# Kernel tuning notes

Measured on AMD Instinct MI355X. Metric: run time of the kernel, lower is better.

The kernel has to match this reference:

```python
import jax, jax.numpy as jnp
import numpy as np


def setup_inputs() -> dict:
    key = jax.random.key(0)
    k1, k2, k3 = jax.random.split(key, 3)
    B, D, L = 32768, 1024, 2
    return {
        "x": jax.random.normal(k1, (B, D), dtype=jnp.float32),
        "local_angles": jax.random.normal(k2, (L, D), dtype=jnp.float32),
        "ent_angles": jax.random.normal(k3, (L, D // 2), dtype=jnp.float32),
    }


def _local_layer(out, angles):
    # Sequential chain of Givens rotations on column pairs (i, (i+1)%D).
    # Each step uses the already-updated columns, exactly like the torch loop
    # (out = out @ R.T  ==  rotate columns i and j of out).
    D = out.shape[1]
    idx = jnp.arange(D)

    def body(o, inp):
        i, theta = inp
        j = (i + 1) % D
        c, s = jnp.cos(theta), jnp.sin(theta)
        ci = jnp.take(o, i, axis=1)  # [B]
        cj = jnp.take(o, j, axis=1)  # [B]
        o = o.at[:, i].set(c * ci - s * cj)
        o = o.at[:, j].set(s * ci + c * cj)
        return o, None

    out, _ = jax.lax.scan(body, out, (idx, angles))
    return out


def _ent_layer(out, angles):
    # Entangler rotations act on disjoint pairs (2k, 2k+1) -> fully vectorized.
    B, D = out.shape
    p = out.reshape(B, D // 2, 2)
    c, s = jnp.cos(angles), jnp.sin(angles)  # [D//2]
    x0, x1 = p[..., 0], p[..., 1]
    return jnp.stack([c * x0 - s * x1, s * x0 + c * x1], axis=-1).reshape(B, D)


def reference(x, local_angles, ent_angles):
    out = x
    num_layers = local_angles.shape[0]
    for l in range(num_layers):
        out = _local_layer(out, local_angles[l])
        out = _ent_layer(out, ent_angles[l])
    return out
```

## Files before the change

### kernel.cpp

```cpp
#include <hip/hip_runtime.h>

#define D_DIM    1024
#define PER_LANE 16
#define NLAYER   2
#define NPAIR    8
#define WPB      4
#define ROWS_PW  8
#define NBUF     4

typedef float nf4 __attribute__((ext_vector_type(4)));

__device__ __forceinline__ int swz(int c) { return c ^ ((c >> 3) & 7); }

template<int CTRL, int RMASK>
__device__ __forceinline__ float dpp_mov(float src, float oldv) {
    return __int_as_float(__builtin_amdgcn_update_dpp(
        __float_as_int(oldv), __float_as_int(src), CTRL, RMASK, 0xF, false));
}

__global__ void angles_kernel(const float* __restrict__ la,
                              const float* __restrict__ ea,
                              float* __restrict__ tab) {
    int t  = blockIdx.x * blockDim.x + threadIdx.x;
    int nt = gridDim.x * blockDim.x;
    for (int i = t; i < NLAYER * D_DIM; i += nt) {
        float s, c; sincosf(la[i], &s, &c);
        tab[i] = c; tab[2048 + i] = s;
    }
    for (int i = t; i < NLAYER * (D_DIM / 2); i += nt) {
        float s, c; sincosf(ea[i], &s, &c);
        tab[4096 + i] = c; tab[5120 + i] = s;
    }
}

__global__ __launch_bounds__(256) void qent_kernel(
        const float* __restrict__ x,
        const float* __restrict__ tab,
        float* __restrict__ out, int B)
{
    const int lane  = threadIdx.x & 63;
    const int wid   = threadIdx.x >> 6;
    const int gwave = blockIdx.x * WPB + wid;

    __shared__ float4 tb[WPB][NBUF][256];
    __shared__ float2 lds_ces[NLAYER][NPAIR][64];

    for (int t = threadIdx.x; t < NLAYER * 512; t += 256) {
        int L = t >> 9, p = t & 511;
        int m = p >> 6, ln = p & 63;
        float2 cs;
        cs.x = tab[4096 + L * 512 + ln * 8 + m];
        cs.y = tab[5120 + L * 512 + ln * 8 + m];
        lds_ces[L][m][ln] = cs;
    }
    __syncthreads();

    float cl[NLAYER][PER_LANE], sl[NLAYER][PER_LANE];
    #pragma unroll
    for (int L = 0; L < NLAYER; ++L) {
        const float4* cp = reinterpret_cast<const float4*>(tab + L * D_DIM + lane * PER_LANE);
        const float4* sp = reinterpret_cast<const float4*>(tab + 2048 + L * D_DIM + lane * PER_LANE);
        #pragma unroll
        for (int q = 0; q < 4; ++q) {
            float4 c4 = cp[q], s4 = sp[q];
            cl[L][4*q+0] = c4.x; cl[L][4*q+1] = c4.y; cl[L][4*q+2] = c4.z; cl[L][4*q+3] = c4.w;
            sl[L][4*q+0] = s4.x; sl[L][4*q+1] = s4.y; sl[L][4*q+2] = s4.z; sl[L][4*q+3] = s4.w;
        }
    }

    const int l2 = lane ^ (lane >> 3);
    auto stage = [&](int b, int row) {
        const float* src = x + (size_t)row * D_DIM;
        #pragma unroll
        for (int q = 0; q < 4; ++q) {
            __builtin_amdgcn_global_load_lds(
                (const __attribute__((address_space(1))) void*)(src + q * 256 + l2 * 4),
                (__attribute__((address_space(3))) void*)&tb[wid][b][q * 64],
                16, 0, 0);
        }
    };

    const int row0 = gwave * ROWS_PW;
    stage(0, row0 + 0);
    stage(1, row0 + 1);
    stage(2, row0 + 2);

    for (int it = 0; it < ROWS_PW; ++it) {
        const int cur = it & (NBUF - 1);

        if (it + 3 < ROWS_PW) stage((it + 3) & (NBUF - 1), row0 + it + 3);

        if      (it == 0)           asm volatile("s_waitcnt vmcnt(12)" ::: "memory");
        else if (it == 1)           asm volatile("s_waitcnt vmcnt(16)" ::: "memory");
        else if (it == 2)           asm volatile("s_waitcnt vmcnt(20)" ::: "memory");
        else if (it <= ROWS_PW - 4) asm volatile("s_waitcnt vmcnt(24)" ::: "memory");
        else if (it == ROWS_PW - 3) asm volatile("s_waitcnt vmcnt(20)" ::: "memory");
        else if (it == ROWS_PW - 2) asm volatile("s_waitcnt vmcnt(16)" ::: "memory");
        else                        asm volatile("s_waitcnt vmcnt(12)" ::: "memory");

        float v[PER_LANE];
        #pragma unroll
        for (int r = 0; r < 4; ++r) {
            float4 t = tb[wid][cur][swz(4 * lane + r)];
            v[4*r+0] = t.x; v[4*r+1] = t.y; v[4*r+2] = t.z; v[4*r+3] = t.w;
        }

        #pragma unroll
        for (int L = 0; L < NLAYER; ++L) {
            float vnf = dpp_mov<0x130, 0xF>(v[0], v[0]);

            float A = 1.f, Bv = 0.f;
            #pragma unroll
            for (int k = 0; k < PER_LANE; ++k) {
                float vn = (k < PER_LANE - 1) ? v[k + 1] : vnf;
                Bv = sl[L][k] * Bv + cl[L][k] * vn;
                A  = sl[L][k] * A;
            }

            float Ai = A, Bi = Bv;
            #define SCAN_STEP(CTRL, RMASK) do {                   \
                float Au = dpp_mov<CTRL, RMASK>(Ai, 1.0f);        \
                float Bu = dpp_mov<CTRL, RMASK>(Bi, 0.0f);        \
                Bi = fmaf(Ai, Bu, Bi);                            \
                Ai *= Au; } while (0)
            SCAN_STEP(0x111, 0xF);
            SCAN_STEP(0x112, 0xF);
            SCAN_STEP(0x114, 0xF);
            SCAN_STEP(0x118, 0xF);
            SCAN_STEP(0x142, 0xA);
            SCAN_STEP(0x143, 0xC);
            #undef SCAN_STEP

            float Ax = dpp_mov<0x138, 0xF>(Ai, 0.0f);
            float Bx = dpp_mov<0x138, 0xF>(Bi, 0.0f);
            float v0b = __int_as_float(
                __builtin_amdgcn_readfirstlane(__float_as_int(v[0])));
            float u   = (lane == 0) ? v[0] : fmaf(Ax, v0b, Bx);

            #pragma unroll
            for (int k = 0; k < PER_LANE - 1; ++k) {
                float vn = v[k + 1];
                float f  = cl[L][k] * u - sl[L][k] * vn;
                u        = sl[L][k] * u + cl[L][k] * vn;
                v[k] = f;
            }
            float a0 = __int_as_float(
                __builtin_amdgcn_readfirstlane(__float_as_int(v[0])));
            float vn15 = (lane == 63) ? a0 : vnf;
            float f15  = cl[L][PER_LANE-1] * u - sl[L][PER_LANE-1] * vn15;
            float un   = sl[L][PER_LANE-1] * u + cl[L][PER_LANE-1] * vn15;
            v[PER_LANE-1] = f15;
            float f0new = __int_as_float(
                __builtin_amdgcn_readlane(__float_as_int(un), 63));
            v[0] = (lane == 0) ? f0new : v[0];

            #pragma unroll
            for (int m = 0; m < NPAIR; ++m) {
                float2 cs = lds_ces[L][m][lane];
                float x0 = v[2*m], x1 = v[2*m+1];
                v[2*m]   = cs.x * x0 - cs.y * x1;
                v[2*m+1] = cs.y * x0 + cs.x * x1;
            }
        }

        #pragma unroll
        for (int r = 0; r < 4; ++r) {
            float4 t;
            t.x = v[4*r+0]; t.y = v[4*r+1]; t.z = v[4*r+2]; t.w = v[4*r+3];
            tb[wid][cur][swz(4 * lane + r)] = t;
        }
        nf4* op = reinterpret_cast<nf4*>(out + (size_t)(row0 + it) * D_DIM);
        #pragma unroll
        for (int q = 0; q < 4; ++q) {
            float4 t = tb[wid][cur][swz(q * 64 + lane)];
            nf4 w; w.x = t.x; w.y = t.y; w.z = t.z; w.w = t.w;
            __builtin_nontemporal_store(w, &op[q * 64 + lane]);
        }
    }
}

extern "C" void kernel_launch(void* const* d_in, const int* in_sizes, int n_in,
                              void* d_out, int out_size, void* d_ws, size_t ws_size,
                              hipStream_t stream) {
    const float* x  = (const float*)d_in[0];
    const float* la = (const float*)d_in[1];
    const float* ea = (const float*)d_in[2];
    float* out = (float*)d_out;
    float* tab = (float*)d_ws;
    int B = in_sizes[0] / D_DIM;

    angles_kernel<<<64, 256, 0, stream>>>(la, ea, tab);
    qent_kernel<<<1024, 256, 0, stream>>>(x, tab, out, B);
}
```

Baseline: 55.00 us.

## Replace async global-to-LDS 4-deep pipeline with register prefetch of next row

Drops the global_load_lds four-buffer staging and its hand-written vmcnt waits. Each wave now loads the next row into registers while computing the current one, then writes it into a single input LDS buffer, with a separate output LDS buffer for the transpose on store. This simplifies synchronisation and shrinks LDS use, which could raise occupancy. In exchange, prefetch depth falls from three rows to one and the load data must pass through VGPRs, adding register pressure and leaving less memory latency hidden.

Result: slower. 58.25 us (+5.9%).

```diff
diff --git a/kernel.cpp b/kernel.cpp
--- a/kernel.cpp
+++ b/kernel.cpp
@@ -6,7 +6,6 @@
 #define NPAIR    8
 #define WPB      4
 #define ROWS_PW  8
-#define NBUF     4
 
 typedef float nf4 __attribute__((ext_vector_type(4)));
 
@@ -42,7 +41,8 @@
     const int wid   = threadIdx.x >> 6;
     const int gwave = blockIdx.x * WPB + wid;
 
-    __shared__ float4 tb[WPB][NBUF][256];
+    __shared__ float4 ibuf[WPB][256];
+    __shared__ float4 obuf[WPB][256];
     __shared__ float2 lds_ces[NLAYER][NPAIR][64];
 
     for (int t = threadIdx.x; t < NLAYER * 512; t += 256) {
@@ -68,40 +68,27 @@
         }
     }
 
-    const int l2 = lane ^ (lane >> 3);
-    auto stage = [&](int b, int row) {
-        const float* src = x + (size_t)row * D_DIM;
+    const int row0 = gwave * ROWS_PW;
+
+    {
+        const float4* rp = reinterpret_cast<const float4*>(x + (size_t)row0 * D_DIM);
         #pragma unroll
-        for (int q = 0; q < 4; ++q) {
-            __builtin_amdgcn_global_load_lds(
-                (const __attribute__((address_space(1))) void*)(src + q * 256 + l2 * 4),
-                (__attribute__((address_space(3))) void*)&tb[wid][b][q * 64],
-                16, 0, 0);
-        }
-    };
-
-    const int row0 = gwave * ROWS_PW;
-    stage(0, row0 + 0);
-    stage(1, row0 + 1);
-    stage(2, row0 + 2);
+        for (int q = 0; q < 4; ++q) ibuf[wid][swz(q * 64 + lane)] = rp[q * 64 + lane];
+    }
 
     for (int it = 0; it < ROWS_PW; ++it) {
-        const int cur = it & (NBUF - 1);
-
-        if (it + 3 < ROWS_PW) stage((it + 3) & (NBUF - 1), row0 + it + 3);
-
-        if      (it == 0)           asm volatile("s_waitcnt vmcnt(12)" ::: "memory");
-        else if (it == 1)           asm volatile("s_waitcnt vmcnt(16)" ::: "memory");
-        else if (it == 2)           asm volatile("s_waitcnt vmcnt(20)" ::: "memory");
-        else if (it <= ROWS_PW - 4) asm volatile("s_waitcnt vmcnt(24)" ::: "memory");
-        else if (it == ROWS_PW - 3) asm volatile("s_waitcnt vmcnt(20)" ::: "memory");
-        else if (it == ROWS_PW - 2) asm volatile("s_waitcnt vmcnt(16)" ::: "memory");
-        else                        asm volatile("s_waitcnt vmcnt(12)" ::: "memory");
+        float4 nxt[4];
+        if (it + 1 < ROWS_PW) {
+            const float4* rp =
+                reinterpret_cast<const float4*>(x + (size_t)(row0 + it + 1) * D_DIM);
+            #pragma unroll
+            for (int q = 0; q < 4; ++q) nxt[q] = rp[q * 64 + lane];
+        }
 
         float v[PER_LANE];
         #pragma unroll
         for (int r = 0; r < 4; ++r) {
-            float4 t = tb[wid][cur][swz(4 * lane + r)];
+            float4 t = ibuf[wid][swz(4 * lane + r)];
             v[4*r+0] = t.x; v[4*r+1] = t.y; v[4*r+2] = t.z; v[4*r+3] = t.w;
         }
 
@@ -163,16 +150,21 @@
             }
         }
 
+        if (it + 1 < ROWS_PW) {
+            #pragma unroll
+            for (int q = 0; q < 4; ++q) ibuf[wid][swz(q * 64 + lane)] = nxt[q];
+        }
+
         #pragma unroll
         for (int r = 0; r < 4; ++r) {
             float4 t;
             t.x = v[4*r+0]; t.y = v[4*r+1]; t.z = v[4*r+2]; t.w = v[4*r+3];
-            tb[wid][cur][swz(4 * lane + r)] = t;
+            obuf[wid][swz(4 * lane + r)] = t;
         }
         nf4* op = reinterpret_cast<nf4*>(out + (size_t)(row0 + it) * D_DIM);
         #pragma unroll
         for (int q = 0; q < 4; ++q) {
-            float4 t = tb[wid][cur][swz(q * 64 + lane)];
+            float4 t = obuf[wid][swz(q * 64 + lane)];
             nf4 w; w.x = t.x; w.y = t.y; w.z = t.z; w.w = t.w;
             __builtin_nontemporal_store(w, &op[q * 64 + lane]);
         }
```
